# Performance work log

Measured on AMD Instinct MI355X. Metric: run time of the kernel, lower is better.

Reference implementation:

```python
import jax, jax.numpy as jnp
import numpy as np

ALPHA = 0.2  # leaky-relu negative slope
N_NODES = 50000
IN_F = 256
OUT_F = 64
N_EDGES = 1600000


def setup_inputs() -> dict:
    key = jax.random.key(0)
    k1, k2, k3, k4 = jax.random.split(key, 4)
    x = jax.random.normal(k1, (N_NODES, IN_F), dtype=jnp.float32)
    # xavier_normal-ish scales for params
    W = jax.random.normal(k2, (IN_F, OUT_F), dtype=jnp.float32) * (1.414 * (2.0 / (IN_F + OUT_F)) ** 0.5)
    a = jax.random.normal(k3, (1, 2 * OUT_F), dtype=jnp.float32) * (1.414 * (2.0 / (1 + 2 * OUT_F)) ** 0.5)
    edge_index = jax.random.randint(k4, (2, N_EDGES), 0, N_NODES, dtype=jnp.int64)
    return {"x": x, "W": W, "a": a, "edge_index": edge_index}


def reference(x, W, a, edge_index):
    N = x.shape[0]
    src = edge_index[0]  # row index of sparse adjacency (aggregation target)
    dst = edge_index[1]  # column index (neighbor being gathered)
    h = x @ W  # [N, out]
    out_f = h.shape[1]
    # a @ cat(h[src], h[dst]) == (h @ a1)[src] + (h @ a2)[dst]
    a1 = a[0, :out_f]
    a2 = a[0, out_f:]
    s_src = h @ a1  # [N]
    s_dst = h @ a2  # [N]
    score = s_src[src] + s_dst[dst]  # [E]
    edge_e = jnp.exp(-jax.nn.leaky_relu(score, negative_slope=ALPHA))  # [E]
    # e_rowsum[i] = sum_{e: src==i} edge_e[e]
    e_rowsum = jax.ops.segment_sum(edge_e, src, num_segments=N)  # [N]
    # h_prime[i] = sum_{e: src==i} edge_e[e] * h[dst[e]]
    h_prime = jax.ops.segment_sum(edge_e[:, None] * h[dst], src, num_segments=N)  # [N, out]
    h_prime = h_prime / e_rowsum[:, None]
    return jax.nn.elu(h_prime)
```

## Files before the change

### kernel.cpp

```cpp
#include <hip/hip_runtime.h>
#include <hip/hip_bf16.h>
#include <hip/hip_fp16.h>


#define ALPHA 0.2f
#define KDIM 256
#define FDIM 64
#define BIN_CHUNK 8192
#define BUCKET_CAP 4096
#define HCAP 2304

typedef __bf16 bf16x8 __attribute__((ext_vector_type(8)));
typedef float f32x4 __attribute__((ext_vector_type(4)));
typedef unsigned int u32;
typedef unsigned short u16;

__global__ __launch_bounds__(256) void gat_wt_kernel(
    const float* __restrict__ W, __hip_bfloat16* __restrict__ w_t,
    int* __restrict__ bcur)
{
    const int t = blockIdx.x * 256 + threadIdx.x;
    if (t < KDIM * FDIM) {
        const int k = t >> 6;
        const int n = t & 63;
        w_t[n * KDIM + k] = __float2bfloat16(W[t]);
    }
    if (t < 1024) bcur[t] = 0;
}

__global__ __launch_bounds__(256) void gat_gemm_bin_kernel(
    const float* __restrict__ x, const __hip_bfloat16* __restrict__ w_tp,
    const float* __restrict__ a, __hip_bfloat16* __restrict__ h_bf,
    float* __restrict__ s_src, float* __restrict__ s_dst,
    const int* __restrict__ srcA, const int* __restrict__ dstA,
    int* __restrict__ bcur, u32* __restrict__ pair,
    int N, int E, int NBU, int NBLK)
{
    __shared__ int hist[1024];
    __shared__ int lcur[1024];

    const int t = threadIdx.x;

    if ((int)blockIdx.x < NBLK) {
        for (int j = t; j < 1024; j += 256) hist[j] = 0;
        __syncthreads();
        const int base = blockIdx.x * BIN_CHUNK;
        const int cnt = min(BIN_CHUNK, E - base);
        for (int i = t; i < cnt; i += 256)
            atomicAdd(&hist[srcA[base + i] >> 6], 1);
        __syncthreads();
        for (int j = t; j < NBU; j += 256) {
            const int v = hist[j];
            lcur[j] = v ? (j * BUCKET_CAP + atomicAdd(&bcur[j], v)) : 0;
        }
        __syncthreads();
        for (int i = t; i < cnt; i += 256) {
            const int s = srcA[base + i];
            const int d = dstA[base + i];
            const int pos = atomicAdd(&lcur[s >> 6], 1);
            pair[pos] = ((u32)(s & 63) << 16) | (u32)d;
        }
        return;
    }

    const int gb = (int)blockIdx.x - NBLK;
    const int lane = t & 63;
    const int wv = t >> 6;
    const int m0 = gb * 64 + wv * 16;
    const int c = lane & 15;
    const int q = lane >> 4;

    const int r0 = m0 + c;
    const float* xp0 = x + (long)(r0 < N ? r0 : N - 1) * KDIM;
    const __bf16* wt = (const __bf16*)w_tp;

    f32x4 acc[4];
#pragma unroll
    for (int ct = 0; ct < 4; ++ct) acc[ct] = (f32x4){0.f, 0.f, 0.f, 0.f};

#pragma unroll 2
    for (int kc = 0; kc < 8; ++kc) {
        const int k0 = kc * 32 + q * 8;
        const float4 xa0 = *(const float4*)(xp0 + k0);
        const float4 xb0 = *(const float4*)(xp0 + k0 + 4);
        bf16x8 af0;
        af0[0] = (__bf16)xa0.x; af0[1] = (__bf16)xa0.y;
        af0[2] = (__bf16)xa0.z; af0[3] = (__bf16)xa0.w;
        af0[4] = (__bf16)xb0.x; af0[5] = (__bf16)xb0.y;
        af0[6] = (__bf16)xb0.z; af0[7] = (__bf16)xb0.w;
#pragma unroll
        for (int ct = 0; ct < 4; ++ct) {
            const bf16x8 bf = *(const bf16x8*)(wt + (ct * 16 + c) * KDIM + k0);
            acc[ct] = __builtin_amdgcn_mfma_f32_16x16x32_bf16(af0, bf, acc[ct], 0, 0, 0);
        }
    }

    float a1c[4], a2c[4];
#pragma unroll
    for (int ct = 0; ct < 4; ++ct) {
        a1c[ct] = a[ct * 16 + c];
        a2c[ct] = a[FDIM + ct * 16 + c];
    }

    float s1r[4], s2r[4];
#pragma unroll
    for (int reg = 0; reg < 4; ++reg) {
        float s1 = 0.f, s2 = 0.f;
#pragma unroll
        for (int ct = 0; ct < 4; ++ct) {
            s1 += acc[ct][reg] * a1c[ct];
            s2 += acc[ct][reg] * a2c[ct];
        }
        s1r[reg] = s1; s2r[reg] = s2;
    }
#pragma unroll
    for (int off = 1; off < 16; off <<= 1) {
#pragma unroll
        for (int reg = 0; reg < 4; ++reg) {
            s1r[reg] += __shfl_xor(s1r[reg], off);
            s2r[reg] += __shfl_xor(s2r[reg], off);
        }
    }
#pragma unroll
    for (int reg = 0; reg < 4; ++reg) {
        const int row = m0 + q * 4 + reg;
        if (row < N) {
#pragma unroll
            for (int ct = 0; ct < 4; ++ct)
                h_bf[(long)row * FDIM + ct * 16 + c] = __float2bfloat16(acc[ct][reg]);
            if (c == 0) { s_src[row] = s1r[reg]; s_dst[row] = s2r[reg]; }
        }
    }
}

__global__ __launch_bounds__(256) void gat_sortgather_kernel(
    const u32* __restrict__ pair, const int* __restrict__ bcur,
    const float* __restrict__ s_src, const float* __restrict__ s_dst,
    const __hip_bfloat16* __restrict__ h_bf, float* __restrict__ out, int N)
{
    __shared__ u32 slds[HCAP];
    __shared__ int cur[32];
    __shared__ int nst[32];
    __shared__ int nen[32];
    __shared__ float ssl[32];

    const int b = (int)blockIdx.x >> 1;
    const int hf = (int)blockIdx.x & 1;
    const int t = threadIdx.x;
    const int s0 = (b << 6) + (hf << 5);
    const int abase = b * BUCKET_CAP;
    const int n = min(bcur[b], BUCKET_CAP);

    if (t < 32) {
        cur[t] = 0;
        ssl[t] = (s0 + t < N) ? s_src[s0 + t] : 0.f;
    }
    __syncthreads();
    for (int i = t; i < n; i += 256) {
        const int sl = (int)(pair[abase + i] >> 16);
        if ((sl >> 5) == hf) atomicAdd(&cur[sl & 31], 1);
    }
    __syncthreads();
    if (t < 32) {
        const int v = cur[t];
        int incl = v;
#pragma unroll
        for (int off = 1; off < 32; off <<= 1) {
            const int nv = __shfl_up(incl, off);
            if (t >= off) incl += nv;
        }
        const int excl = incl - v;
        nst[t] = excl;
        nen[t] = min(excl + v, HCAP);
        cur[t] = excl;
    }
    __syncthreads();
    for (int i = t; i < n; i += 256) {
        const u32 p = pair[abase + i];
        const int sl = (int)(p >> 16);
        if ((sl >> 5) != hf) continue;
        const int d = (int)(p & 0xFFFFu);
        const int slot = atomicAdd(&cur[sl & 31], 1);
        if (slot < HCAP) {
            const float sc = ssl[sl & 31] + s_dst[d];
            const float lr = sc > 0.f ? sc : ALPHA * sc;
            const float wgt = __expf(-lr);
            const u32 wh = (u32)__half_as_ushort(__float2half(wgt));
            slds[slot] = (u32)d | (wh << 16);
        }
    }
    __syncthreads();

    const int wv = t >> 6;
    const int lane = t & 63;
    const int q = lane >> 3;
    const int c = lane & 7;
    const __bf16* hb = (const __bf16*)h_bf;

    for (int nl = wv; nl < 32; nl += 4) {
        const int node = s0 + nl;
        if (node >= N) break;
        const int start = nst[nl];
        const int end = nen[nl];

        float acc0[8], acc1[8];
#pragma unroll
        for (int j = 0; j < 8; ++j) { acc0[j] = 0.f; acc1[j] = 0.f; }
        float wsum0 = 0.f, wsum1 = 0.f;

        int e = start + q;
        for (; e + 8 < end; e += 16) {
            const u32 p0 = slds[e];
            const u32 p1 = slds[e + 8];
            const int d0 = (int)(p0 & 0xFFFFu);
            const int d1 = (int)(p1 & 0xFFFFu);
            const bf16x8 hv0 = *(const bf16x8*)(hb + (long)d0 * FDIM + 8 * c);
            const bf16x8 hv1 = *(const bf16x8*)(hb + (long)d1 * FDIM + 8 * c);
            const float w0 = __half2float(__ushort_as_half((u16)(p0 >> 16)));
            const float w1 = __half2float(__ushort_as_half((u16)(p1 >> 16)));
#pragma unroll
            for (int j = 0; j < 8; ++j) {
                acc0[j] += w0 * (float)hv0[j];
                acc1[j] += w1 * (float)hv1[j];
            }
            wsum0 += w0;
            wsum1 += w1;
        }
        if (e < end) {
            const u32 p0 = slds[e];
            const int d0 = (int)(p0 & 0xFFFFu);
            const bf16x8 hv0 = *(const bf16x8*)(hb + (long)d0 * FDIM + 8 * c);
            const float w0 = __half2float(__ushort_as_half((u16)(p0 >> 16)));
#pragma unroll
            for (int j = 0; j < 8; ++j) acc0[j] += w0 * (float)hv0[j];
            wsum0 += w0;
        }

        float acc[8];
#pragma unroll
        for (int j = 0; j < 8; ++j) acc[j] = acc0[j] + acc1[j];
        float wsum = wsum0 + wsum1;

#pragma unroll
        for (int off = 8; off < 64; off <<= 1) {
#pragma unroll
            for (int j = 0; j < 8; ++j) acc[j] += __shfl_xor(acc[j], off);
            wsum += __shfl_xor(wsum, off);
        }

        if (q == 0) {
            const float inv = 1.0f / wsum;
            float o[8];
#pragma unroll
            for (int j = 0; j < 8; ++j) {
                const float v = acc[j] * inv;
                o[j] = v > 0.f ? v : expm1f(v);
            }
            float* op = &out[(long)node * FDIM + 8 * c];
            *(float4*)op = make_float4(o[0], o[1], o[2], o[3]);
            *(float4*)(op + 4) = make_float4(o[4], o[5], o[6], o[7]);
        }
    }
}

extern "C" void kernel_launch(void* const* d_in, const int* in_sizes, int n_in,
                              void* d_out, int out_size, void* d_ws, size_t ws_size,
                              hipStream_t stream) {
    const float* x = (const float*)d_in[0];
    const float* W = (const float*)d_in[1];
    const float* a = (const float*)d_in[2];
    const int* ei  = (const int*)d_in[3];

    const int N = in_sizes[0] / KDIM;
    const int E = in_sizes[3] / 2;
    const int NBU = (N + 63) >> 6;
    const int NBLK = (E + BIN_CHUNK - 1) / BIN_CHUNK;
    const int GB = (N + 63) / 64;
    const int* srcA = ei;
    const int* dstA = ei + E;

    __hip_bfloat16* h_bf = (__hip_bfloat16*)d_ws;
    __hip_bfloat16* w_t  = h_bf + (size_t)N * FDIM;
    float* s_src = (float*)(w_t + KDIM * FDIM);
    float* s_dst = s_src + N;
    int* bcur    = (int*)(s_dst + N);
    u32* pair    = (u32*)(bcur + 1024);
    float* out   = (float*)d_out;

    gat_wt_kernel<<<dim3((KDIM * FDIM + 255) / 256), dim3(256), 0, stream>>>(
        W, w_t, bcur);

    gat_gemm_bin_kernel<<<dim3(NBLK + GB), dim3(256), 0, stream>>>(
        x, w_t, a, h_bf, s_src, s_dst, srcA, dstA, bcur, pair, N, E, NBU, NBLK);

    gat_sortgather_kernel<<<dim3(NBU * 2), dim3(256), 0, stream>>>(
        pair, bcur, s_src, s_dst, h_bf, out, N);
}
```

Measured before the change: 179.0 us.

## Fuse W transpose into GEMM via padded LDS staging, replace prep kernel with memset

Removes the separate W-transpose/bf16-convert kernel. Each GEMM block now loads W from global, converts it to bf16 and stores it transposed into padded shared memory, which is unioned with the binning histograms. The bucket cursor reset becomes a hipMemsetAsync, and the k-loop unroll goes from 2 to 4. This saves one kernel launch and reads B fragments from LDS, but every one of ~782 GEMM blocks now redoes the 64KB fp32 W load and conversion, and the larger LDS footprint may reduce occupancy.

After: 171.7 us (median of 2 runs). 4.0% less time.

```diff
diff --git a/kernel.cpp b/kernel.cpp
--- a/kernel.cpp
+++ b/kernel.cpp
@@ -6,6 +6,7 @@
 #define ALPHA 0.2f
 #define KDIM 256
 #define FDIM 64
+#define WPAD 8
 #define BIN_CHUNK 8192
 #define BUCKET_CAP 4096
 #define HCAP 2304
@@ -15,53 +16,50 @@
 typedef unsigned int u32;
 typedef unsigned short u16;
 
-__global__ __launch_bounds__(256) void gat_wt_kernel(
-    const float* __restrict__ W, __hip_bfloat16* __restrict__ w_t,
-    int* __restrict__ bcur)
-{
-    const int t = blockIdx.x * 256 + threadIdx.x;
-    if (t < KDIM * FDIM) {
-        const int k = t >> 6;
-        const int n = t & 63;
-        w_t[n * KDIM + k] = __float2bfloat16(W[t]);
-    }
-    if (t < 1024) bcur[t] = 0;
-}
+union SmemA {
+    struct { int hist[1024]; int lcur[1024]; } bin;
+    __bf16 w[FDIM * (KDIM + WPAD)];
+};
 
 __global__ __launch_bounds__(256) void gat_gemm_bin_kernel(
-    const float* __restrict__ x, const __hip_bfloat16* __restrict__ w_tp,
+    const float* __restrict__ x, const float* __restrict__ W,
     const float* __restrict__ a, __hip_bfloat16* __restrict__ h_bf,
     float* __restrict__ s_src, float* __restrict__ s_dst,
     const int* __restrict__ srcA, const int* __restrict__ dstA,
     int* __restrict__ bcur, u32* __restrict__ pair,
     int N, int E, int NBU, int NBLK)
 {
-    __shared__ int hist[1024];
-    __shared__ int lcur[1024];
-
+    __shared__ SmemA sm;
     const int t = threadIdx.x;
 
     if ((int)blockIdx.x < NBLK) {
-        for (int j = t; j < 1024; j += 256) hist[j] = 0;
+        for (int j = t; j < 1024; j += 256) sm.bin.hist[j] = 0;
         __syncthreads();
         const int base = blockIdx.x * BIN_CHUNK;
         const int cnt = min(BIN_CHUNK, E - base);
         for (int i = t; i < cnt; i += 256)
-            atomicAdd(&hist[srcA[base + i] >> 6], 1);
+            atomicAdd(&sm.bin.hist[srcA[base + i] >> 6], 1);
         __syncthreads();
         for (int j = t; j < NBU; j += 256) {
-            const int v = hist[j];
-            lcur[j] = v ? (j * BUCKET_CAP + atomicAdd(&bcur[j], v)) : 0;
+            const int v = sm.bin.hist[j];
+            sm.bin.lcur[j] = v ? (j * BUCKET_CAP + atomicAdd(&bcur[j], v)) : 0;
         }
         __syncthreads();
         for (int i = t; i < cnt; i += 256) {
             const int s = srcA[base + i];
             const int d = dstA[base + i];
-            const int pos = atomicAdd(&lcur[s >> 6], 1);
+            const int pos = atomicAdd(&sm.bin.lcur[s >> 6], 1);
             pair[pos] = ((u32)(s & 63) << 16) | (u32)d;
         }
         return;
     }
+
+    for (int i = t; i < KDIM * FDIM; i += 256) {
+        const int k = i >> 6;
+        const int n = i & 63;
+        sm.w[n * (KDIM + WPAD) + k] = (__bf16)W[i];
+    }
+    __syncthreads();
 
     const int gb = (int)blockIdx.x - NBLK;
     const int lane = t & 63;
@@ -72,13 +70,12 @@
 
     const int r0 = m0 + c;
     const float* xp0 = x + (long)(r0 < N ? r0 : N - 1) * KDIM;
-    const __bf16* wt = (const __bf16*)w_tp;
 
     f32x4 acc[4];
 #pragma unroll
     for (int ct = 0; ct < 4; ++ct) acc[ct] = (f32x4){0.f, 0.f, 0.f, 0.f};
 
-#pragma unroll 2
+#pragma unroll 4
     for (int kc = 0; kc < 8; ++kc) {
         const int k0 = kc * 32 + q * 8;
         const float4 xa0 = *(const float4*)(xp0 + k0);
@@ -90,7 +87,7 @@
         af0[6] = (__bf16)xb0.z; af0[7] = (__bf16)xb0.w;
 #pragma unroll
         for (int ct = 0; ct < 4; ++ct) {
-            const bf16x8 bf = *(const bf16x8*)(wt + (ct * 16 + c) * KDIM + k0);
+            const bf16x8 bf = *(const bf16x8*)(&sm.w[(ct * 16 + c) * (KDIM + WPAD) + k0]);
             acc[ct] = __builtin_amdgcn_mfma_f32_16x16x32_bf16(af0, bf, acc[ct], 0, 0, 0);
         }
     }
@@ -280,18 +277,16 @@
     const int* dstA = ei + E;
 
     __hip_bfloat16* h_bf = (__hip_bfloat16*)d_ws;
-    __hip_bfloat16* w_t  = h_bf + (size_t)N * FDIM;
-    float* s_src = (float*)(w_t + KDIM * FDIM);
+    float* s_src = (float*)(h_bf + (size_t)N * FDIM);
     float* s_dst = s_src + N;
     int* bcur    = (int*)(s_dst + N);
     u32* pair    = (u32*)(bcur + 1024);
     float* out   = (float*)d_out;
 
-    gat_wt_kernel<<<dim3((KDIM * FDIM + 255) / 256), dim3(256), 0, stream>>>(
-        W, w_t, bcur);
+    hipMemsetAsync(bcur, 0, 1024 * sizeof(int), stream);
 
     gat_gemm_bin_kernel<<<dim3(NBLK + GB), dim3(256), 0, stream>>>(
-        x, w_t, a, h_bf, s_src, s_dst, srcA, dstA, bcur, pair, N, E, NBU, NBLK);
+        x, W, a, h_bf, s_src, s_dst, srcA, dstA, bcur, pair, N, E, NBU, NBLK);
 
     gat_sortgather_kernel<<<dim3(NBU * 2), dim3(256), 0, stream>>>(
         pair, bcur, s_src, s_dst, h_bf, out, N);
```
